# Kernel tuning notes

Measured on AMD Instinct MI355X. Metric: run time of the kernel, lower is better.

The kernel has to match this reference:

```python
import jax, jax.numpy as jnp
import numpy as np

N, DIM, OUT, E = 10000, 256, 256, 320000


def setup_inputs() -> dict:
    key = jax.random.key(0)
    ks = jax.random.split(key, 10)
    def w(k, shape):
        fan_in = shape[0]
        return jax.random.normal(k, shape, jnp.float32) * (fan_in ** -0.5)
    return {
        "v_c": jax.random.normal(ks[0], (N, DIM), jnp.float32),
        # row-normalized-ish random adjacency weights so A @ v stays O(1)
        "A": jax.random.uniform(ks[1], (N, N), jnp.float32) * (2.0 / N),
        "src": jax.random.randint(ks[2], (E,), 0, N, jnp.int32),
        "dst": jax.random.randint(ks[3], (E,), 0, N, jnp.int32),
        # ResidualBlock params: lin1 (dim -> 2dim), lin2 (2dim -> dim)
        "W1": w(ks[4], (DIM, 2 * DIM)), "b1": jnp.zeros((2 * DIM,), jnp.float32),
        "W2": w(ks[5], (2 * DIM, DIM)), "b2": jnp.zeros((DIM,), jnp.float32),
        # LatticeMP_Block lin1 / lin2 (dim -> out_dim)
        "Wl1": w(ks[6], (DIM, OUT)), "bl1": jnp.zeros((OUT,), jnp.float32),
        "Wl2": w(ks[7], (DIM, OUT)), "bl2": jnp.zeros((OUT,), jnp.float32),
    }


def reference(v_c, A, src, dst, W1, b1, W2, b2, Wl1, bl1, Wl2, bl2):
    # ResidualBlock: relu(h + lin2(relu(lin1(h))))
    h1 = jnp.maximum(v_c @ W1 + b1, 0.0) @ W2 + b2          # [N, DIM]
    v = jnp.maximum(v_c + h1, 0.0)                           # [N, DIM]
    # relu(lin1(v)) + relu(lin2(A @ v))
    v = jnp.maximum(v @ Wl1 + bl1, 0.0) + jnp.maximum((A @ v) @ Wl2 + bl2, 0.0)  # [N, OUT]
    # DGL update_all(copy_u, sum): h_N[d] = sum_{(s,d) in E} v[s]
    h_N = jax.ops.segment_sum(v[src], dst, num_segments=N)   # [N, OUT]
    return h_N + v
```

## Files before the change

kernel.cpp:

```cpp
#include <hip/hip_runtime.h>
#include <stdint.h>

#define NN 10000
#define DIMV 256
#define HID 512
#define NEDGE 320000
#define SPLIT 6
#define KCH 1664
#define NKT 313
#define APL 2112
#define ABUF 8448
#define BOFF 16896
#define LDSZ 49664

typedef __attribute__((ext_vector_type(8))) short bf16x8;
typedef __attribute__((ext_vector_type(4))) float f32x4;
typedef __attribute__((ext_vector_type(4))) unsigned short u16x4;
typedef __attribute__((ext_vector_type(2))) unsigned int u32x2;

__device__ __forceinline__ unsigned short f2bf(float f) {
  union { float f; unsigned int u; } c; c.f = f;
  return (unsigned short)((c.u + 0x7FFFu + ((c.u >> 16) & 1u)) >> 16);
}
__device__ __forceinline__ float bf2f(unsigned short h) {
  union { unsigned int u; float f; } c; c.u = ((unsigned int)h) << 16;
  return c.f;
}

__device__ __forceinline__ bf16x8 bzero8() {
  bf16x8 r;
#pragma unroll
  for (int i = 0; i < 8; ++i) r[i] = 0;
  return r;
}

__device__ __forceinline__ bf16x8 pack8(const float* x) {
  bf16x8 r;
#pragma unroll
  for (int i = 0; i < 8; ++i) r[i] = (short)f2bf(x[i]);
  return r;
}

__device__ __forceinline__ u32x2 cvt4v(const f32x4 a) {
  u32x2 r;
  asm("v_cvt_pk_bf16_f32 %0, %1, %2" : "=v"(r[0]) : "v"(a[0]), "v"(a[1]));
  asm("v_cvt_pk_bf16_f32 %0, %1, %2" : "=v"(r[1]) : "v"(a[2]), "v"(a[3]));
  return r;
}

typedef __attribute__((address_space(1))) unsigned int gu32;
typedef __attribute__((address_space(3))) unsigned int lu32;
__device__ __forceinline__ void glds16(const void* g, void* l) {
  __builtin_amdgcn_global_load_lds((const gu32*)g, (lu32*)l, 16, 0, 0);
}

__global__ void k_conv(const float* __restrict__ W1, const float* __restrict__ W2,
                       const float* __restrict__ Wl1, const float* __restrict__ Wl2,
                       unsigned short* __restrict__ W1T, unsigned short* __restrict__ W2T,
                       unsigned short* __restrict__ Wl1T, unsigned short* __restrict__ Wl2T,
                       unsigned short* __restrict__ vB, int* __restrict__ counts) {
  int i = blockIdx.x * 256 + threadIdx.x;
  if (i < 131072) {
    { int k = i >> 9, o = i & 511; W1T[o * 256 + k] = f2bf(W1[i]); }
    { int k = i >> 8, o = i & 255; W2T[o * 512 + k] = f2bf(W2[i]); }
    if (i < 65536) {
      int k = i >> 8, o = i & 255;
      Wl1T[o * 256 + k] = f2bf(Wl1[i]);
      Wl2T[o * 256 + k] = f2bf(Wl2[i]);
    }
    if (i < 4096) {
      int c = i >> 4, kk = 16 + (i & 15);
      int g = kk >> 3;
      int byte = c * 64 + ((g ^ ((c >> 1) & 3)) << 4) + (kk & 7) * 2;
      *(unsigned short*)((char*)vB + (size_t)312 * 16384 + byte) = 0;
    }
    if (i < NN) counts[i] = 0;
  }
}

__launch_bounds__(256, 2)
__global__ void k_mlp(const float* __restrict__ vc,
                      const unsigned short* __restrict__ W1T, const float* __restrict__ b1,
                      const unsigned short* __restrict__ W2T, const float* __restrict__ b2,
                      unsigned short* __restrict__ v_rm, unsigned short* __restrict__ vB,
                      const int* __restrict__ dst, int* __restrict__ counts) {
  if (blockIdx.x >= 313) {
    const int e0 = (blockIdx.x - 313) * 256 + threadIdx.x;
    for (int e = e0; e < NEDGE; e += 40 * 256) atomicAdd(&counts[dst[e]], 1);
    return;
  }
  __shared__ __align__(16) char sm[65536];
  const int t = threadIdx.x;
  const int lane = t & 63, wid = t >> 6;
  const int wr = wid & 1, wc = wid >> 1;
  const int r0 = blockIdx.x * 32;

  {
    const int row = t >> 3, grow = r0 + row;
#pragma unroll
    for (int q = 0; q < 4; ++q) {
      const int slot = (t & 7) * 4 + q;
      float buf[8] = {0.f, 0.f, 0.f, 0.f, 0.f, 0.f, 0.f, 0.f};
      if (grow < NN) {
        const float4 x0 = *(const float4*)(vc + (size_t)grow * DIMV + slot * 8);
        const float4 x1 = *(const float4*)(vc + (size_t)grow * DIMV + slot * 8 + 4);
        buf[0] = x0.x; buf[1] = x0.y; buf[2] = x0.z; buf[3] = x0.w;
        buf[4] = x1.x; buf[5] = x1.y; buf[6] = x1.z; buf[7] = x1.w;
      }
      *(bf16x8*)(sm + row * 512 + ((slot ^ (row & 7)) * 16)) = pack8(buf);
    }
  }

  f32x4 acc1[16];
#pragma unroll
  for (int i = 0; i < 16; ++i) acc1[i] = (f32x4){0.f, 0.f, 0.f, 0.f};

  for (int step = 0; step < 8; ++step) {
    __syncthreads();
#pragma unroll
    for (int rr = 0; rr < 2; ++rr) {
      const int c = t + rr * 256;
      const unsigned short* srcp = W1T + c * 256 + step * 32;
#pragma unroll
      for (int q = 0; q < 4; ++q) {
        bf16x8 w = *(const bf16x8*)(srcp + q * 8);
        *(bf16x8*)(sm + 16384 + c * 64 + ((q ^ ((c >> 1) & 3)) * 16)) = w;
      }
    }
    __syncthreads();
    const int arow = 16 * wr + (lane & 15);
    const int aslot = step * 4 + (lane >> 4);
    const bf16x8 af = *(const bf16x8*)(sm + arow * 512 + ((aslot ^ (arow & 7)) * 16));
#pragma unroll
    for (int ct = 0; ct < 16; ++ct) {
      const int c = 256 * wc + 16 * ct + (lane & 15);
      const bf16x8 bfr =
          *(const bf16x8*)(sm + 16384 + c * 64 + ((((lane >> 4)) ^ ((c >> 1) & 3)) * 16));
      acc1[ct] = __builtin_amdgcn_mfma_f32_16x16x32_bf16(af, bfr, acc1[ct], 0, 0, 0);
    }
  }
  __syncthreads();
#pragma unroll
  for (int ct = 0; ct < 16; ++ct) {
    const int c = 256 * wc + 16 * ct + (lane & 15);
    const float bb = b1[c];
#pragma unroll
    for (int r = 0; r < 4; ++r) {
      const int row = 16 * wr + (lane >> 4) * 4 + r;
      float v = fmaxf(acc1[ct][r] + bb, 0.f);
      const int slot = c >> 3;
      *(unsigned short*)(sm + 16384 + row * 1024 + ((slot ^ (row & 7)) * 16) + (c & 7) * 2) =
          f2bf(v);
    }
  }

  f32x4 acc2[8];
#pragma unroll
  for (int i = 0; i < 8; ++i) acc2[i] = (f32x4){0.f, 0.f, 0.f, 0.f};

  for (int step = 0; step < 16; ++step) {
    __syncthreads();
    {
      const int c = t;
      const unsigned short* srcp = W2T + c * 512 + step * 32;
#pragma unroll
      for (int q = 0; q < 4; ++q) {
        bf16x8 w = *(const bf16x8*)(srcp + q * 8);
        *(bf16x8*)(sm + 49152 + c * 64 + ((q ^ ((c >> 1) & 3)) * 16)) = w;
      }
    }
    __syncthreads();
    const int arow = 16 * wr + (lane & 15);
    const int aslot = step * 4 + (lane >> 4);
    const bf16x8 af = *(const bf16x8*)(sm + 16384 + arow * 1024 + ((aslot ^ (arow & 7)) * 16));
#pragma unroll
    for (int ct = 0; ct < 8; ++ct) {
      const int c = 128 * wc + 16 * ct + (lane & 15);
      const bf16x8 bfr =
          *(const bf16x8*)(sm + 49152 + c * 64 + ((((lane >> 4)) ^ ((c >> 1) & 3)) * 16));
      acc2[ct] = __builtin_amdgcn_mfma_f32_16x16x32_bf16(af, bfr, acc2[ct], 0, 0, 0);
    }
  }

  const int growbase = r0 + 16 * wr + (lane >> 4) * 4;
  if (growbase < NN) {
#pragma unroll
    for (int ct = 0; ct < 8; ++ct) {
      const int c = 128 * wc + 16 * ct + (lane & 15);
      const float bb = b2[c];
      u16x4 pk;
#pragma unroll
      for (int r = 0; r < 4; ++r) {
        const int grow = growbase + r;
        float v = acc2[ct][r] + bb + vc[(size_t)grow * DIMV + c];
        v = fmaxf(v, 0.f);
        const unsigned short hv = f2bf(v);
        v_rm[(size_t)grow * DIMV + c] = hv;
        pk[r] = hv;
      }
      const int tile = growbase >> 5, kk0 = growbase & 31;
      const int g = kk0 >> 3;
      const int byte = c * 64 + ((g ^ ((c >> 1) & 3)) << 4) + (kk0 & 7) * 2;
      *(u16x4*)((char*)vB + (size_t)tile * 16384 + byte) = pk;
    }
  }
}

__launch_bounds__(512, 4)
__global__ void k_av(const float* __restrict__ A, const unsigned short* __restrict__ vB,
                     unsigned short* __restrict__ avpb,
                     const int* __restrict__ counts, int* __restrict__ offsets,
                     int* __restrict__ cursor) {
  __shared__ __align__(16) char sm[LDSZ];
  const int t = threadIdx.x, lane = t & 63, wid = t >> 6;

  if (blockIdx.x >= 474) {
    int* wred = (int*)sm;
    int carry = 0;
    for (int base = 0; base < NN; base += 512) {
      const int i = base + t;
      const int x = (i < NN) ? counts[i] : 0;
      int v = x;
#pragma unroll
      for (int d = 1; d < 64; d <<= 1) {
        int y = __shfl_up(v, d);
        if (lane >= d) v += y;
      }
      if (lane == 63) wred[wid] = v;
      __syncthreads();
      if (t < 8) {
        int sv = wred[t];
#pragma unroll
        for (int d = 1; d < 8; d <<= 1) {
          int y = __shfl_up(sv, d);
          if (t >= d) sv += y;
        }
        wred[t] = sv;
      }
      __syncthreads();
      const int excl = carry + (wid ? wred[wid - 1] : 0) + v - x;
      if (i < NN) { offsets[i] = excl; cursor[i] = excl; }
      carry += wred[7];
      __syncthreads();
    }
    if (t == 0) offsets[NN] = carry;
    return;
  }

  const int wr = wid >> 2, wc = wid & 3;

  const int orig = blockIdx.x;
  const int xcd = orig & 7, idx = orig >> 3;
  const int g = (xcd < 2) ? xcd * 60 + idx : 120 + (xcd - 2) * 59 + idx;
  const int s = g / 79;
  const int xb = g - s * 79;
  const int r0 = xb * 128;
  const int kbase = s * KCH;
  const int tile0 = s * 52;
  const int nst = (s == SPLIT - 1) ? 53 : 52;
  unsigned short* outp = avpb + (size_t)s * NN * DIMV;

  const int srow = t >> 3, sQ = t & 7;
  const float* ap0 = A + (size_t)min(r0 + srow, NN - 1) * NN;
  const float* ap1 = A + (size_t)min(r0 + 64 + srow, NN - 1) * NN;
  const int wbase = (sQ >> 1) * APL + (sQ & 1) * 8;
  const int w0 = wbase + srow * 16;
  const int w1 = wbase + (64 + srow) * 16;

  f32x4 aR0, aR1;

#define AISSUE(ST)                                            \
  do {                                                        \
    int kq = kbase + (ST)*32 + sQ * 4;                        \
    kq = min(kq, 9996);         \
    aR0 = *(const f32x4*)(ap0 + kq);                          \
    aR1 = *(const f32x4*)(ap1 + kq);                          \
  } while (0)

#define AWRITE(BUF)                                           \
  do {                                                        \
    char* wb = sm + (BUF)*ABUF;                               \
    *(u32x2*)(wb + w0) = cvt4v(aR0);                          \
    *(u32x2*)(wb + w1) = cvt4v(aR1);                          \
  } while (0)

#define BSTAGE(BUF, TILE)                                                     \
  do {                                                                        \
    char* lb = sm + BOFF + (BUF)*16384 + wid * 1024;                          \
    const char* gp = (const char*)vB + (size_t)(TILE)*16384 + wid * 1024 +    \
                     lane * 16;                                               \
    glds16(gp, lb);                                                           \
    glds16(gp + 8192, lb + 8192);                                             \
  } while (0)

  f32x4 acc[4][4];
#pragma unroll
  for (int i = 0; i < 4; ++i)
#pragma unroll
    for (int j = 0; j < 4; ++j) acc[i][j] = (f32x4){0.f, 0.f, 0.f, 0.f};

  const int rbase = (lane >> 4) * APL + (wr * 64 + (lane & 15)) * 16;
  int boff[4];
#pragma unroll
  for (int ct = 0; ct < 4; ++ct) {
    const int col = wc * 64 + ct * 16 + (lane & 15);
    boff[ct] = col * 64 + (((lane >> 4) ^ ((col >> 1) & 3)) << 4);
  }

#define COMPUTE(CUR)                                                                 \
  do {                                                                              \
    const char* ab = sm + (CUR)*ABUF;                                               \
    const char* bb = sm + BOFF + (CUR)*16384;                                       \
    const bf16x8 af0 = *(const bf16x8*)(ab + rbase);                                \
    const bf16x8 af1 = *(const bf16x8*)(ab + rbase + 256);                          \
    const bf16x8 af2 = *(const bf16x8*)(ab + rbase + 512);                          \
    const bf16x8 af3 = *(const bf16x8*)(ab + rbase + 768);                          \
    _Pragma("unroll") for (int ct = 0; ct < 4; ++ct) {                              \
      const bf16x8 bfr = *(const bf16x8*)(bb + boff[ct]);                           \
      acc[0][ct] = __builtin_amdgcn_mfma_f32_16x16x32_bf16(af0, bfr, acc[0][ct], 0, 0, 0); \
      acc[1][ct] = __builtin_amdgcn_mfma_f32_16x16x32_bf16(af1, bfr, acc[1][ct], 0, 0, 0); \
      acc[2][ct] = __builtin_amdgcn_mfma_f32_16x16x32_bf16(af2, bfr, acc[2][ct], 0, 0, 0); \
      acc[3][ct] = __builtin_amdgcn_mfma_f32_16x16x32_bf16(af3, bfr, acc[3][ct], 0, 0, 0); \
    }                                                                               \
  } while (0)

  AISSUE(0);
  AWRITE(0);
  BSTAGE(0, tile0);
  __syncthreads();

  int cur = 0;
  for (int st = 0; st < nst; ++st) {
    const bool more = (st + 1 < nst);
    if (more) {
      AISSUE(st + 1);
      BSTAGE(cur ^ 1, tile0 + st + 1);
    }
    COMPUTE(cur);
    if (more) AWRITE(cur ^ 1);
    __syncthreads();
    cur ^= 1;
  }
#undef AISSUE
#undef AWRITE
#undef BSTAGE
#undef COMPUTE

#pragma unroll
  for (int rt = 0; rt < 4; ++rt) {
    const int gb = r0 + wr * 64 + rt * 16 + (lane >> 4) * 4;
    if (gb < NN) {
#pragma unroll
      for (int ct = 0; ct < 4; ++ct) {
        const int col = wc * 64 + ct * 16 + (lane & 15);
#pragma unroll
        for (int r = 0; r < 4; ++r)
          outp[(size_t)(gb + r) * DIMV + col] = f2bf(acc[rt][ct][r]);
      }
    }
  }
}

__launch_bounds__(256, 2)
__global__ void k_out(const unsigned short* __restrict__ v_rm,
                      const unsigned short* __restrict__ avpb,
                      const unsigned short* __restrict__ Wl1T, const float* __restrict__ bl1,
                      const unsigned short* __restrict__ Wl2T, const float* __restrict__ bl2,
                      unsigned short* __restrict__ v2b, float* __restrict__ outb,
                      const int* __restrict__ src, const int* __restrict__ dst,
                      int* __restrict__ cursor, int* __restrict__ srcbuf) {
  if (blockIdx.x >= 313) {
    const int e0 = (blockIdx.x - 313) * 256 + threadIdx.x;
    for (int e = e0; e < NEDGE; e += 40 * 256) {
      const int pos = atomicAdd(&cursor[dst[e]], 1);
      srcbuf[pos] = src[e];
    }
    return;
  }
  __shared__ __align__(16) char sm[65536];
  const int t = threadIdx.x, lane = t & 63, wid = t >> 6;
  const int wr = wid & 1, wc = wid >> 1;
  const int r0 = blockIdx.x * 32;

  {
    const int row = t >> 3, grow = r0 + row;
#pragma unroll
    for (int q = 0; q < 4; ++q) {
      const int slot = (t & 7) * 4 + q;
      bf16x8 w = (grow < NN) ? *(const bf16x8*)(v_rm + (size_t)grow * DIMV + slot * 8) : bzero8();
      *(bf16x8*)(sm + row * 512 + ((slot ^ (row & 7)) * 16)) = w;
    }
#pragma unroll
    for (int q = 0; q < 4; ++q) {
      const int slot = (t & 7) * 4 + q;
      float buf[8] = {0.f, 0.f, 0.f, 0.f, 0.f, 0.f, 0.f, 0.f};
      if (grow < NN) {
#pragma unroll
        for (int p = 0; p < SPLIT; ++p) {
          const bf16x8 a =
              *(const bf16x8*)(avpb + (size_t)p * NN * DIMV + (size_t)grow * DIMV + slot * 8);
#pragma unroll
          for (int z = 0; z < 8; ++z) buf[z] += bf2f((unsigned short)a[z]);
        }
      }
      *(bf16x8*)(sm + 16384 + row * 512 + ((slot ^ (row & 7)) * 16)) = pack8(buf);
    }
  }

  f32x4 acc1[8], acc2[8];
#pragma unroll
  for (int i = 0; i < 8; ++i) {
    acc1[i] = (f32x4){0.f, 0.f, 0.f, 0.f};
    acc2[i] = (f32x4){0.f, 0.f, 0.f, 0.f};
  }

  for (int step = 0; step < 8; ++step) {
    __syncthreads();
    {
      const int c = t;
      const unsigned short* s1 = Wl1T + c * 256 + step * 32;
      const unsigned short* s2 = Wl2T + c * 256 + step * 32;
#pragma unroll
      for (int q = 0; q < 4; ++q) {
        const int ps = (q ^ ((c >> 1) & 3)) * 16;
        *(bf16x8*)(sm + 32768 + c * 64 + ps) = *(const bf16x8*)(s1 + q * 8);
        *(bf16x8*)(sm + 49152 + c * 64 + ps) = *(const bf16x8*)(s2 + q * 8);
      }
    }
    __syncthreads();
    const int arow = 16 * wr + (lane & 15);
    const int aslot = step * 4 + (lane >> 4);
    const bf16x8 a1 = *(const bf16x8*)(sm + arow * 512 + ((aslot ^ (arow & 7)) * 16));
    const bf16x8 a2 = *(const bf16x8*)(sm + 16384 + arow * 512 + ((aslot ^ (arow & 7)) * 16));
#pragma unroll
    for (int ct = 0; ct < 8; ++ct) {
      const int c = 128 * wc + 16 * ct + (lane & 15);
      const int bs = (((lane >> 4)) ^ ((c >> 1) & 3)) * 16;
      acc1[ct] = __builtin_amdgcn_mfma_f32_16x16x32_bf16(
          a1, *(const bf16x8*)(sm + 32768 + c * 64 + bs), acc1[ct], 0, 0, 0);
      acc2[ct] = __builtin_amdgcn_mfma_f32_16x16x32_bf16(
          a2, *(const bf16x8*)(sm + 49152 + c * 64 + bs), acc2[ct], 0, 0, 0);
    }
  }

  const int growbase = r0 + 16 * wr + (lane >> 4) * 4;
  if (growbase < NN) {
#pragma unroll
    for (int ct = 0; ct < 8; ++ct) {
      const int c = 128 * wc + 16 * ct + (lane & 15);
      const float u1 = bl1[c], u2 = bl2[c];
#pragma unroll
      for (int r = 0; r < 4; ++r) {
        const float x = fmaxf(acc1[ct][r] + u1, 0.f) + fmaxf(acc2[ct][r] + u2, 0.f);
        v2b[(size_t)(growbase + r) * DIMV + c] = f2bf(x);
        outb[(size_t)(growbase + r) * DIMV + c] = x;
      }
    }
  }
}

__launch_bounds__(256)
__global__ void k_gather(const unsigned short* __restrict__ v2b,
                         const int* __restrict__ offsets,
                         const int* __restrict__ srcbuf, float* __restrict__ outb) {
  const int n = (blockIdx.x * 256 + threadIdx.x) >> 6;
  if (n >= NN) return;
  const int lane = threadIdx.x & 63;
  const int beg = offsets[n], end = offsets[n + 1];
  float4 a0 = {0.f, 0.f, 0.f, 0.f}, a1 = a0, a2 = a0, a3 = a0;
  float4 a4 = a0, a5 = a0, a6 = a0, a7 = a0;
  int j = beg;
  for (; j + 8 <= end; j += 8) {
    const int s0 = srcbuf[j], s1 = srcbuf[j + 1], s2 = srcbuf[j + 2], s3 = srcbuf[j + 3];
    const int s4 = srcbuf[j + 4], s5 = srcbuf[j + 5], s6 = srcbuf[j + 6], s7 = srcbuf[j + 7];
    const u16x4 x0 = *(const u16x4*)(v2b + (size_t)s0 * DIMV + lane * 4);
    const u16x4 x1 = *(const u16x4*)(v2b + (size_t)s1 * DIMV + lane * 4);
    const u16x4 x2 = *(const u16x4*)(v2b + (size_t)s2 * DIMV + lane * 4);
    const u16x4 x3 = *(const u16x4*)(v2b + (size_t)s3 * DIMV + lane * 4);
    const u16x4 x4 = *(const u16x4*)(v2b + (size_t)s4 * DIMV + lane * 4);
    const u16x4 x5 = *(const u16x4*)(v2b + (size_t)s5 * DIMV + lane * 4);
    const u16x4 x6 = *(const u16x4*)(v2b + (size_t)s6 * DIMV + lane * 4);
    const u16x4 x7 = *(const u16x4*)(v2b + (size_t)s7 * DIMV + lane * 4);
    a0.x += bf2f(x0[0]); a0.y += bf2f(x0[1]); a0.z += bf2f(x0[2]); a0.w += bf2f(x0[3]);
    a1.x += bf2f(x1[0]); a1.y += bf2f(x1[1]); a1.z += bf2f(x1[2]); a1.w += bf2f(x1[3]);
    a2.x += bf2f(x2[0]); a2.y += bf2f(x2[1]); a2.z += bf2f(x2[2]); a2.w += bf2f(x2[3]);
    a3.x += bf2f(x3[0]); a3.y += bf2f(x3[1]); a3.z += bf2f(x3[2]); a3.w += bf2f(x3[3]);
    a4.x += bf2f(x4[0]); a4.y += bf2f(x4[1]); a4.z += bf2f(x4[2]); a4.w += bf2f(x4[3]);
    a5.x += bf2f(x5[0]); a5.y += bf2f(x5[1]); a5.z += bf2f(x5[2]); a5.w += bf2f(x5[3]);
    a6.x += bf2f(x6[0]); a6.y += bf2f(x6[1]); a6.z += bf2f(x6[2]); a6.w += bf2f(x6[3]);
    a7.x += bf2f(x7[0]); a7.y += bf2f(x7[1]); a7.z += bf2f(x7[2]); a7.w += bf2f(x7[3]);
  }
  for (; j < end; ++j) {
    const int s0 = srcbuf[j];
    const u16x4 x0 = *(const u16x4*)(v2b + (size_t)s0 * DIMV + lane * 4);
    a0.x += bf2f(x0[0]); a0.y += bf2f(x0[1]); a0.z += bf2f(x0[2]); a0.w += bf2f(x0[3]);
  }
  a0.x += a1.x + a2.x + a3.x + a4.x + a5.x + a6.x + a7.x;
  a0.y += a1.y + a2.y + a3.y + a4.y + a5.y + a6.y + a7.y;
  a0.z += a1.z + a2.z + a3.z + a4.z + a5.z + a6.z + a7.z;
  a0.w += a1.w + a2.w + a3.w + a4.w + a5.w + a6.w + a7.w;
  float* o = outb + (size_t)n * DIMV + lane * 4;
  float4 cur = *(const float4*)o;
  cur.x += a0.x; cur.y += a0.y; cur.z += a0.z; cur.w += a0.w;
  *(float4*)o = cur;
}

extern "C" void kernel_launch(void* const* d_in, const int* in_sizes, int n_in,
                              void* d_out, int out_size, void* d_ws, size_t ws_size,
                              hipStream_t stream) {
  const float* vc  = (const float*)d_in[0];
  const float* A   = (const float*)d_in[1];
  const int*   src = (const int*)d_in[2];
  const int*   dst = (const int*)d_in[3];
  const float* W1  = (const float*)d_in[4];
  const float* b1  = (const float*)d_in[5];
  const float* W2  = (const float*)d_in[6];
  const float* b2  = (const float*)d_in[7];
  const float* Wl1 = (const float*)d_in[8];
  const float* bl1 = (const float*)d_in[9];
  const float* Wl2 = (const float*)d_in[10];
  const float* bl2 = (const float*)d_in[11];
  float* outb = (float*)d_out;
  char* ws = (char*)d_ws;

  unsigned short* W1T  = (unsigned short*)(ws + 0);
  unsigned short* W2T  = (unsigned short*)(ws + 262144);
  unsigned short* Wl1T = (unsigned short*)(ws + 524288);
  unsigned short* Wl2T = (unsigned short*)(ws + 655360);
  unsigned short* vB   = (unsigned short*)(ws + 786432);
  unsigned short* v_rm = (unsigned short*)(ws + 5914624);
  int* counts  = (int*)(ws + 11034624);
  int* offsets = (int*)(ws + 11075584);
  int* cursor  = (int*)(ws + 11116544);
  int* srcbuf  = (int*)(ws + 11157504);
  unsigned short* avpb = (unsigned short*)(ws + 12437760);
  unsigned short* v2b  = (unsigned short*)(ws + 43157760);

  hipLaunchKernelGGL(k_conv, dim3(512), dim3(256), 0, stream,
                     W1, W2, Wl1, Wl2, W1T, W2T, Wl1T, Wl2T, vB, counts);
  hipLaunchKernelGGL(k_mlp, dim3(353), dim3(256), 0, stream,
                     vc, W1T, b1, W2T, b2, v_rm, vB, dst, counts);
  hipLaunchKernelGGL(k_av, dim3(475), dim3(512), 0, stream,
                     A, vB, avpb, counts, offsets, cursor);
  hipLaunchKernelGGL(k_out, dim3(353), dim3(256), 0, stream,
                     v_rm, avpb, Wl1T, bl1, Wl2T, bl2, v2b, outb,
                     src, dst, cursor, srcbuf);
  hipLaunchKernelGGL(k_gather, dim3((NN * 64 + 255) / 256), dim3(256), 0, stream,
                     v2b, offsets, srcbuf, outb);
}
```

Baseline: 236.6 us.

## Stage fp32 A tiles via direct-to-LDS loads with triple buffering in A@v GEMM

The A@v kernel now loads fp32 A tiles straight into LDS with global_load_lds (XOR-swizzled) and converts them to bf16 at fragment-read time, instead of loading into registers and writing converted values. It switches to a 3-stage ring buffer with explicit vmcnt waits and raw barriers. Row tiles shrink from 128 to 64, doubling the block count to 942 with a matching XCD remap. The aim is to hide the HBM stream of A better and drop register staging, at the cost of more LDS per block (72KB), reading A from LDS in fp32, and halving MFMA reuse per B fragment.

```diff
diff --git a/kernel.cpp b/kernel.cpp
--- a/kernel.cpp
+++ b/kernel.cpp
@@ -8,10 +8,8 @@
 #define SPLIT 6
 #define KCH 1664
 #define NKT 313
-#define APL 2112
-#define ABUF 8448
-#define BOFF 16896
-#define LDSZ 49664
+#define BUFSZ 24576
+#define NGEMM 942
 
 typedef __attribute__((ext_vector_type(8))) short bf16x8;
 typedef __attribute__((ext_vector_type(4))) float f32x4;
@@ -41,11 +39,13 @@
   return r;
 }
 
-__device__ __forceinline__ u32x2 cvt4v(const f32x4 a) {
-  u32x2 r;
-  asm("v_cvt_pk_bf16_f32 %0, %1, %2" : "=v"(r[0]) : "v"(a[0]), "v"(a[1]));
-  asm("v_cvt_pk_bf16_f32 %0, %1, %2" : "=v"(r[1]) : "v"(a[2]), "v"(a[3]));
-  return r;
+__device__ __forceinline__ bf16x8 cvt8v(const f32x4 a, const f32x4 b) {
+  union { unsigned int u[4]; bf16x8 v; } r;
+  asm("v_cvt_pk_bf16_f32 %0, %1, %2" : "=v"(r.u[0]) : "v"(a[0]), "v"(a[1]));
+  asm("v_cvt_pk_bf16_f32 %0, %1, %2" : "=v"(r.u[1]) : "v"(a[2]), "v"(a[3]));
+  asm("v_cvt_pk_bf16_f32 %0, %1, %2" : "=v"(r.u[2]) : "v"(b[0]), "v"(b[1]));
+  asm("v_cvt_pk_bf16_f32 %0, %1, %2" : "=v"(r.u[3]) : "v"(b[2]), "v"(b[3]));
+  return r.v;
 }
 
 typedef __attribute__((address_space(1))) unsigned int gu32;
@@ -211,10 +211,10 @@
                      unsigned short* __restrict__ avpb,
                      const int* __restrict__ counts, int* __restrict__ offsets,
                      int* __restrict__ cursor) {
-  __shared__ __align__(16) char sm[LDSZ];
+  __shared__ __align__(16) char sm[73728];
   const int t = threadIdx.x, lane = t & 63, wid = t >> 6;
 
-  if (blockIdx.x >= 474) {
+  if (blockIdx.x >= NGEMM) {
     int* wred = (int*)sm;
     int carry = 0;
     for (int base = 0; base < NN; base += 512) {
@@ -251,104 +251,90 @@
 
   const int orig = blockIdx.x;
   const int xcd = orig & 7, idx = orig >> 3;
-  const int g = (xcd < 2) ? xcd * 60 + idx : 120 + (xcd - 2) * 59 + idx;
-  const int s = g / 79;
-  const int xb = g - s * 79;
-  const int r0 = xb * 128;
+  const int g = (xcd < 6) ? xcd * 118 + idx : 708 + (xcd - 6) * 117 + idx;
+  const int s = g / 157;
+  const int xb = g - s * 157;
+  const int r0 = xb * 64;
   const int kbase = s * KCH;
   const int tile0 = s * 52;
   const int nst = (s == SPLIT - 1) ? 53 : 52;
   unsigned short* outp = avpb + (size_t)s * NN * DIMV;
 
-  const int srow = t >> 3, sQ = t & 7;
-  const float* ap0 = A + (size_t)min(r0 + srow, NN - 1) * NN;
-  const float* ap1 = A + (size_t)min(r0 + 64 + srow, NN - 1) * NN;
-  const int wbase = (sQ >> 1) * APL + (sQ & 1) * 8;
-  const int w0 = wbase + srow * 16;
-  const int w1 = wbase + (64 + srow) * 16;
-
-  f32x4 aR0, aR1;
-
-#define AISSUE(ST)                                            \
-  do {                                                        \
-    int kq = kbase + (ST)*32 + sQ * 4;                        \
-    kq = min(kq, 9996);         \
-    aR0 = *(const f32x4*)(ap0 + kq);                          \
-    aR1 = *(const f32x4*)(ap1 + kq);                          \
+  const int arow_t = wid * 8 + (lane >> 3);
+  const int ac4 = ((lane & 7) ^ (lane >> 3)) * 4;
+  const float* abase_g = A + (size_t)min(r0 + arow_t, NN - 1) * NN;
+
+#define GSTAGE(BI, ST)                                                         \
+  do {                                                                         \
+    char* la_ = sm + (BI)*BUFSZ + wid * 1024;                                  \
+    const float* ga_ = abase_g + min(kbase + (ST)*32 + ac4, 9996);             \
+    glds16(ga_, la_);                                                          \
+    char* lb_ = sm + (BI)*BUFSZ + 8192 + wid * 1024;                           \
+    const char* gb_ =                                                          \
+        (const char*)vB + (size_t)(tile0 + (ST)) * 16384 + wid * 1024 + lane * 16; \
+    glds16(gb_, lb_);                                                          \
+    glds16(gb_ + 8192, lb_ + 8192);                                            \
   } while (0)
 
-#define AWRITE(BUF)                                           \
-  do {                                                        \
-    char* wb = sm + (BUF)*ABUF;                               \
-    *(u32x2*)(wb + w0) = cvt4v(aR0);                          \
-    *(u32x2*)(wb + w1) = cvt4v(aR1);                          \
-  } while (0)
-
-#define BSTAGE(BUF, TILE)                                                     \
-  do {                                                                        \
-    char* lb = sm + BOFF + (BUF)*16384 + wid * 1024;                          \
-    const char* gp = (const char*)vB + (size_t)(TILE)*16384 + wid * 1024 +    \
-                     lane * 16;                                               \
-    glds16(gp, lb);                                                           \
-    glds16(gp + 8192, lb + 8192);                                             \
-  } while (0)
-
-  f32x4 acc[4][4];
-#pragma unroll
-  for (int i = 0; i < 4; ++i)
+  f32x4 acc[2][4];
+#pragma unroll
+  for (int i = 0; i < 2; ++i)
 #pragma unroll
     for (int j = 0; j < 4; ++j) acc[i][j] = (f32x4){0.f, 0.f, 0.f, 0.f};
 
-  const int rbase = (lane >> 4) * APL + (wr * 64 + (lane & 15)) * 16;
+  const int frow = wr * 32 + (lane & 15);
+  const int kg = lane >> 4;
   int boff[4];
 #pragma unroll
   for (int ct = 0; ct < 4; ++ct) {
     const int col = wc * 64 + ct * 16 + (lane & 15);
-    boff[ct] = col * 64 + (((lane >> 4) ^ ((col >> 1) & 3)) << 4);
-  }
-
-#define COMPUTE(CUR)                                                                 \
-  do {                                                                              \
-    const char* ab = sm + (CUR)*ABUF;                                               \
-    const char* bb = sm + BOFF + (CUR)*16384;                                       \
-    const bf16x8 af0 = *(const bf16x8*)(ab + rbase);                                \
-    const bf16x8 af1 = *(const bf16x8*)(ab + rbase + 256);                          \
-    const bf16x8 af2 = *(const bf16x8*)(ab + rbase + 512);                          \
-    const bf16x8 af3 = *(const bf16x8*)(ab + rbase + 768);                          \
-    _Pragma("unroll") for (int ct = 0; ct < 4; ++ct) {                              \
-      const bf16x8 bfr = *(const bf16x8*)(bb + boff[ct]);                           \
+    boff[ct] = 8192 + col * 64 + ((kg ^ ((col >> 1) & 3)) << 4);
+  }
+
+#define COMPUTE(BI)                                                            \
+  do {                                                                         \
+    const char* bb_ = sm + (BI)*BUFSZ;                                         \
+    const int rw_ = frow & 7;                                                  \
+    const bf16x8 af0 = cvt8v(                                                  \
+        *(const f32x4*)(bb_ + frow * 128 + (((kg * 2) ^ rw_) << 4)),           \
+        *(const f32x4*)(bb_ + frow * 128 + (((kg * 2 + 1) ^ rw_) << 4)));      \
+    const bf16x8 af1 = cvt8v(                                                  \
+        *(const f32x4*)(bb_ + (frow + 16) * 128 + (((kg * 2) ^ rw_) << 4)),    \
+        *(const f32x4*)(bb_ + (frow + 16) * 128 + (((kg * 2 + 1) ^ rw_) << 4)));\
+    _Pragma("unroll") for (int ct = 0; ct < 4; ++ct) {                         \
+      const bf16x8 bfr = *(const bf16x8*)(bb_ + boff[ct]);                     \
       acc[0][ct] = __builtin_amdgcn_mfma_f32_16x16x32_bf16(af0, bfr, acc[0][ct], 0, 0, 0); \
       acc[1][ct] = __builtin_amdgcn_mfma_f32_16x16x32_bf16(af1, bfr, acc[1][ct], 0, 0, 0); \
-      acc[2][ct] = __builtin_amdgcn_mfma_f32_16x16x32_bf16(af2, bfr, acc[2][ct], 0, 0, 0); \
-      acc[3][ct] = __builtin_amdgcn_mfma_f32_16x16x32_bf16(af3, bfr, acc[3][ct], 0, 0, 0); \
-    }                                                                               \
+    }                                                                          \
   } while (0)
 
-  AISSUE(0);
-  AWRITE(0);
-  BSTAGE(0, tile0);
-  __syncthreads();
+  GSTAGE(0, 0);
+  GSTAGE(1, 1);
 
   int cur = 0;
   for (int st = 0; st < nst; ++st) {
-    const bool more = (st + 1 < nst);
-    if (more) {
-      AISSUE(st + 1);
-      BSTAGE(cur ^ 1, tile0 + st + 1);
-    }
+    if (st + 2 < nst) {
+      int sb = cur + 2; if (sb >= 3) sb -= 3;
+      GSTAGE(sb, st + 2);
+    }
+    __builtin_amdgcn_sched_barrier(0);
+    const int ahead = nst - 1 - st;
+    if (ahead >= 2)      asm volatile("s_waitcnt vmcnt(6)" ::: "memory");
+    else if (ahead == 1) asm volatile("s_waitcnt vmcnt(3)" ::: "memory");
+    else                 asm volatile("s_waitcnt vmcnt(0)" ::: "memory");
+    __builtin_amdgcn_sched_barrier(0);
+    __builtin_amdgcn_s_barrier();
     COMPUTE(cur);
-    if (more) AWRITE(cur ^ 1);
-    __syncthreads();
-    cur ^= 1;
-  }
-#undef AISSUE
-#undef AWRITE
-#undef BSTAGE
+    __builtin_amdgcn_sched_barrier(0);
+    __builtin_amdgcn_s_barrier();
+    ++cur; if (cur >= 3) cur = 0;
+  }
+#undef GSTAGE
 #undef COMPUTE
 
 #pragma unroll
-  for (int rt = 0; rt < 4; ++rt) {
-    const int gb = r0 + wr * 64 + rt * 16 + (lane >> 4) * 4;
+  for (int rt = 0; rt < 2; ++rt) {
+    const int gb = r0 + wr * 32 + rt * 16 + (lane >> 4) * 4;
     if (gb < NN) {
 #pragma unroll
       for (int ct = 0; ct < 4; ++ct) {
@@ -540,7 +526,7 @@
                      W1, W2, Wl1, Wl2, W1T, W2T, Wl1T, Wl2T, vB, counts);
   hipLaunchKernelGGL(k_mlp, dim3(353), dim3(256), 0, stream,
                      vc, W1T, b1, W2T, b2, v_rm, vB, dst, counts);
-  hipLaunchKernelGGL(k_av, dim3(475), dim3(512), 0, stream,
+  hipLaunchKernelGGL(k_av, dim3(NGEMM + 1), dim3(512), 0, stream,
                      A, vB, avpb, counts, offsets, cursor);
   hipLaunchKernelGGL(k_out, dim3(353), dim3(256), 0, stream,
                      v_rm, avpb, Wl1T, bl1, Wl2T, bl2, v2b, outb,
```

After: 257.5 us. +8.8%, slower.

## Prefetch A-tile global loads two stages ahead with register double-buffering

Applied to the files above, without the earlier changes.

The A-operand global loads in the split-K GEMM now go into two alternating register sets and are issued two stages ahead of use, instead of one. Explicit s_waitcnt vmcnt(2) plus a raw s_barrier replace __syncthreads, so the newest A loads can stay in flight across the barrier. This is meant to hide HBM latency on the streaming reads of the large A matrix. The cost is extra VGPRs and fragile hand-written wait counts that assume the compiler's memory-op ordering.

```diff
diff --git a/kernel.cpp b/kernel.cpp
--- a/kernel.cpp
+++ b/kernel.cpp
@@ -267,21 +267,31 @@
   const int w0 = wbase + srow * 16;
   const int w1 = wbase + (64 + srow) * 16;
 
-  f32x4 aR0, aR1;
-
-#define AISSUE(ST)                                            \
+  f32x4 aR0, aR1, bR0, bR1;
+
+#define AISSUE_A(ST)                                          \
   do {                                                        \
-    int kq = kbase + (ST)*32 + sQ * 4;                        \
-    kq = min(kq, 9996);         \
+    int kq = min(kbase + (ST)*32 + sQ * 4, 9996);             \
     aR0 = *(const f32x4*)(ap0 + kq);                          \
     aR1 = *(const f32x4*)(ap1 + kq);                          \
   } while (0)
-
-#define AWRITE(BUF)                                           \
+#define AISSUE_B(ST)                                          \
+  do {                                                        \
+    int kq = min(kbase + (ST)*32 + sQ * 4, 9996);             \
+    bR0 = *(const f32x4*)(ap0 + kq);                          \
+    bR1 = *(const f32x4*)(ap1 + kq);                          \
+  } while (0)
+#define AWRITE_A(BUF)                                         \
   do {                                                        \
     char* wb = sm + (BUF)*ABUF;                               \
     *(u32x2*)(wb + w0) = cvt4v(aR0);                          \
     *(u32x2*)(wb + w1) = cvt4v(aR1);                          \
+  } while (0)
+#define AWRITE_B(BUF)                                         \
+  do {                                                        \
+    char* wb = sm + (BUF)*ABUF;                               \
+    *(u32x2*)(wb + w0) = cvt4v(bR0);                          \
+    *(u32x2*)(wb + w1) = cvt4v(bR1);                          \
   } while (0)
 
 #define BSTAGE(BUF, TILE)                                                     \
@@ -307,42 +317,57 @@
     boff[ct] = col * 64 + (((lane >> 4) ^ ((col >> 1) & 3)) << 4);
   }
 
-#define COMPUTE(CUR)                                                                 \
-  do {                                                                              \
-    const char* ab = sm + (CUR)*ABUF;                                               \
-    const char* bb = sm + BOFF + (CUR)*16384;                                       \
-    const bf16x8 af0 = *(const bf16x8*)(ab + rbase);                                \
-    const bf16x8 af1 = *(const bf16x8*)(ab + rbase + 256);                          \
-    const bf16x8 af2 = *(const bf16x8*)(ab + rbase + 512);                          \
-    const bf16x8 af3 = *(const bf16x8*)(ab + rbase + 768);                          \
-    _Pragma("unroll") for (int ct = 0; ct < 4; ++ct) {                              \
-      const bf16x8 bfr = *(const bf16x8*)(bb + boff[ct]);                           \
+#define COMPUTE(CUR)                                                               \
+  do {                                                                            \
+    const char* ab = sm + (CUR)*ABUF;                                             \
+    const char* bb = sm + BOFF + (CUR)*16384;                                     \
+    const bf16x8 af0 = *(const bf16x8*)(ab + rbase);                              \
+    const bf16x8 af1 = *(const bf16x8*)(ab + rbase + 256);                        \
+    const bf16x8 af2 = *(const bf16x8*)(ab + rbase + 512);                        \
+    const bf16x8 af3 = *(const bf16x8*)(ab + rbase + 768);                        \
+    _Pragma("unroll") for (int ct = 0; ct < 4; ++ct) {                            \
+      const bf16x8 bfr = *(const bf16x8*)(bb + boff[ct]);                         \
       acc[0][ct] = __builtin_amdgcn_mfma_f32_16x16x32_bf16(af0, bfr, acc[0][ct], 0, 0, 0); \
       acc[1][ct] = __builtin_amdgcn_mfma_f32_16x16x32_bf16(af1, bfr, acc[1][ct], 0, 0, 0); \
       acc[2][ct] = __builtin_amdgcn_mfma_f32_16x16x32_bf16(af2, bfr, acc[2][ct], 0, 0, 0); \
       acc[3][ct] = __builtin_amdgcn_mfma_f32_16x16x32_bf16(af3, bfr, acc[3][ct], 0, 0, 0); \
-    }                                                                               \
+    }                                                                             \
   } while (0)
 
-  AISSUE(0);
-  AWRITE(0);
+  AISSUE_A(0);
+  AWRITE_A(0);
   BSTAGE(0, tile0);
-  __syncthreads();
+  AISSUE_B(1);
+  __builtin_amdgcn_sched_barrier(0);
+  asm volatile("s_waitcnt lgkmcnt(0)" ::: "memory");
+  asm volatile("s_waitcnt vmcnt(2)" ::: "memory");
+  __builtin_amdgcn_sched_barrier(0);
+  __builtin_amdgcn_s_barrier();
 
   int cur = 0;
   for (int st = 0; st < nst; ++st) {
     const bool more = (st + 1 < nst);
+    const bool more2 = (st + 2 < nst);
+    if (more) BSTAGE(cur ^ 1, tile0 + st + 1);
+    if (more2) {
+      if ((st & 1) == 0) AISSUE_A(st + 2); else AISSUE_B(st + 2);
+    }
+    COMPUTE(cur);
     if (more) {
-      AISSUE(st + 1);
-      BSTAGE(cur ^ 1, tile0 + st + 1);
-    }
-    COMPUTE(cur);
-    if (more) AWRITE(cur ^ 1);
-    __syncthreads();
+      if ((st & 1) == 0) AWRITE_B(cur ^ 1); else AWRITE_A(cur ^ 1);
+    }
+    __builtin_amdgcn_sched_barrier(0);
+    asm volatile("s_waitcnt lgkmcnt(0)" ::: "memory");
+    if (more2) asm volatile("s_waitcnt vmcnt(2)" ::: "memory");
+    else       asm volatile("s_waitcnt vmcnt(0)" ::: "memory");
+    __builtin_amdgcn_sched_barrier(0);
+    __builtin_amdgcn_s_barrier();
     cur ^= 1;
   }
-#undef AISSUE
-#undef AWRITE
+#undef AISSUE_A
+#undef AISSUE_B
+#undef AWRITE_A
+#undef AWRITE_B
 #undef BSTAGE
 #undef COMPUTE
 
```

New measurement: 239.5 us. Within noise of the previous version (+1.2%).

## Pre-tile weights into MFMA fragment order and read B operands directly from global

Applied to the files above, without the earlier changes.

The weight conversion kernel now writes W1/W2/Wl1/Wl2 in a k-tiled, fragment-contiguous layout so each lane's 16-byte MFMA B operand sits contiguously in global memory. The MLP and post-aggregation kernels then load B fragments straight from global/L2 instead of staging them through LDS each k-step. This removes two barriers per step and shrinks LDS use, which may raise occupancy. The trade-off is exposed global-load latency on every MFMA operand, with no LDS reuse across waves.

```diff
diff --git a/kernel.cpp b/kernel.cpp
--- a/kernel.cpp
+++ b/kernel.cpp
@@ -61,12 +61,19 @@
                        unsigned short* __restrict__ vB, int* __restrict__ counts) {
   int i = blockIdx.x * 256 + threadIdx.x;
   if (i < 131072) {
-    { int k = i >> 9, o = i & 511; W1T[o * 256 + k] = f2bf(W1[i]); }
-    { int k = i >> 8, o = i & 255; W2T[o * 512 + k] = f2bf(W2[i]); }
+    {
+      int tile = i >> 14, o = (i >> 5) & 511, kk = i & 31;
+      W1T[i] = f2bf(W1[(size_t)(tile * 32 + kk) * 512 + o]);
+    }
+    {
+      int tile = i >> 13, o = (i >> 5) & 255, kk = i & 31;
+      W2T[i] = f2bf(W2[(size_t)(tile * 32 + kk) * 256 + o]);
+    }
     if (i < 65536) {
-      int k = i >> 8, o = i & 255;
-      Wl1T[o * 256 + k] = f2bf(Wl1[i]);
-      Wl2T[o * 256 + k] = f2bf(Wl2[i]);
+      int tile = i >> 13, o = (i >> 5) & 255, kk = i & 31;
+      int srci = (tile * 32 + kk) * 256 + o;
+      Wl1T[i] = f2bf(Wl1[srci]);
+      Wl2T[i] = f2bf(Wl2[srci]);
     }
     if (i < 4096) {
       int c = i >> 4, kk = 16 + (i & 15);
@@ -89,7 +96,7 @@
     for (int e = e0; e < NEDGE; e += 40 * 256) atomicAdd(&counts[dst[e]], 1);
     return;
   }
-  __shared__ __align__(16) char sm[65536];
+  __shared__ __align__(16) char sm[49152];
   const int t = threadIdx.x;
   const int lane = t & 63, wid = t >> 6;
   const int wr = wid & 1, wc = wid >> 1;
@@ -110,36 +117,26 @@
       *(bf16x8*)(sm + row * 512 + ((slot ^ (row & 7)) * 16)) = pack8(buf);
     }
   }
+  __syncthreads();
 
   f32x4 acc1[16];
 #pragma unroll
   for (int i = 0; i < 16; ++i) acc1[i] = (f32x4){0.f, 0.f, 0.f, 0.f};
 
+#pragma unroll 1
   for (int step = 0; step < 8; ++step) {
-    __syncthreads();
-#pragma unroll
-    for (int rr = 0; rr < 2; ++rr) {
-      const int c = t + rr * 256;
-      const unsigned short* srcp = W1T + c * 256 + step * 32;
-#pragma unroll
-      for (int q = 0; q < 4; ++q) {
-        bf16x8 w = *(const bf16x8*)(srcp + q * 8);
-        *(bf16x8*)(sm + 16384 + c * 64 + ((q ^ ((c >> 1) & 3)) * 16)) = w;
-      }
-    }
-    __syncthreads();
     const int arow = 16 * wr + (lane & 15);
     const int aslot = step * 4 + (lane >> 4);
     const bf16x8 af = *(const bf16x8*)(sm + arow * 512 + ((aslot ^ (arow & 7)) * 16));
+    const unsigned short* wb = W1T + step * 16384 + (lane & 15) * 32 + (lane >> 4) * 8;
 #pragma unroll
     for (int ct = 0; ct < 16; ++ct) {
-      const int c = 256 * wc + 16 * ct + (lane & 15);
-      const bf16x8 bfr =
-          *(const bf16x8*)(sm + 16384 + c * 64 + ((((lane >> 4)) ^ ((c >> 1) & 3)) * 16));
+      const int c0 = 256 * wc + 16 * ct;
+      const bf16x8 bfr = *(const bf16x8*)(wb + c0 * 32);
       acc1[ct] = __builtin_amdgcn_mfma_f32_16x16x32_bf16(af, bfr, acc1[ct], 0, 0, 0);
     }
   }
-  __syncthreads();
+
 #pragma unroll
   for (int ct = 0; ct < 16; ++ct) {
     const int c = 256 * wc + 16 * ct + (lane & 15);
@@ -153,31 +150,22 @@
           f2bf(v);
     }
   }
+  __syncthreads();
 
   f32x4 acc2[8];
 #pragma unroll
   for (int i = 0; i < 8; ++i) acc2[i] = (f32x4){0.f, 0.f, 0.f, 0.f};
 
+#pragma unroll 1
   for (int step = 0; step < 16; ++step) {
-    __syncthreads();
-    {
-      const int c = t;
-      const unsigned short* srcp = W2T + c * 512 + step * 32;
-#pragma unroll
-      for (int q = 0; q < 4; ++q) {
-        bf16x8 w = *(const bf16x8*)(srcp + q * 8);
-        *(bf16x8*)(sm + 49152 + c * 64 + ((q ^ ((c >> 1) & 3)) * 16)) = w;
-      }
-    }
-    __syncthreads();
     const int arow = 16 * wr + (lane & 15);
     const int aslot = step * 4 + (lane >> 4);
     const bf16x8 af = *(const bf16x8*)(sm + 16384 + arow * 1024 + ((aslot ^ (arow & 7)) * 16));
+    const unsigned short* wb = W2T + step * 8192 + (lane & 15) * 32 + (lane >> 4) * 8;
 #pragma unroll
     for (int ct = 0; ct < 8; ++ct) {
-      const int c = 128 * wc + 16 * ct + (lane & 15);
-      const bf16x8 bfr =
-          *(const bf16x8*)(sm + 49152 + c * 64 + ((((lane >> 4)) ^ ((c >> 1) & 3)) * 16));
+      const int c0 = 128 * wc + 16 * ct;
+      const bf16x8 bfr = *(const bf16x8*)(wb + c0 * 32);
       acc2[ct] = __builtin_amdgcn_mfma_f32_16x16x32_bf16(af, bfr, acc2[ct], 0, 0, 0);
     }
   }
@@ -271,8 +259,7 @@
 
 #define AISSUE(ST)                                            \
   do {                                                        \
-    int kq = kbase + (ST)*32 + sQ * 4;                        \
-    kq = min(kq, 9996);         \
+    int kq = min(kbase + (ST)*32 + sQ * 4, 9996);             \
     aR0 = *(const f32x4*)(ap0 + kq);                          \
     aR1 = *(const f32x4*)(ap1 + kq);                          \
   } while (0)
@@ -307,21 +294,21 @@
     boff[ct] = col * 64 + (((lane >> 4) ^ ((col >> 1) & 3)) << 4);
   }
 
-#define COMPUTE(CUR)                                                                 \
-  do {                                                                              \
-    const char* ab = sm + (CUR)*ABUF;                                               \
-    const char* bb = sm + BOFF + (CUR)*16384;                                       \
-    const bf16x8 af0 = *(const bf16x8*)(ab + rbase);                                \
-    const bf16x8 af1 = *(const bf16x8*)(ab + rbase + 256);                          \
-    const bf16x8 af2 = *(const bf16x8*)(ab + rbase + 512);                          \
-    const bf16x8 af3 = *(const bf16x8*)(ab + rbase + 768);                          \
-    _Pragma("unroll") for (int ct = 0; ct < 4; ++ct) {                              \
-      const bf16x8 bfr = *(const bf16x8*)(bb + boff[ct]);                           \
+#define COMPUTE(CUR)                                                               \
+  do {                                                                            \
+    const char* ab = sm + (CUR)*ABUF;                                             \
+    const char* bb = sm + BOFF + (CUR)*16384;                                     \
+    const bf16x8 af0 = *(const bf16x8*)(ab + rbase);                              \
+    const bf16x8 af1 = *(const bf16x8*)(ab + rbase + 256);                        \
+    const bf16x8 af2 = *(const bf16x8*)(ab + rbase + 512);                        \
+    const bf16x8 af3 = *(const bf16x8*)(ab + rbase + 768);                        \
+    _Pragma("unroll") for (int ct = 0; ct < 4; ++ct) {                            \
+      const bf16x8 bfr = *(const bf16x8*)(bb + boff[ct]);                         \
       acc[0][ct] = __builtin_amdgcn_mfma_f32_16x16x32_bf16(af0, bfr, acc[0][ct], 0, 0, 0); \
       acc[1][ct] = __builtin_amdgcn_mfma_f32_16x16x32_bf16(af1, bfr, acc[1][ct], 0, 0, 0); \
       acc[2][ct] = __builtin_amdgcn_mfma_f32_16x16x32_bf16(af2, bfr, acc[2][ct], 0, 0, 0); \
       acc[3][ct] = __builtin_amdgcn_mfma_f32_16x16x32_bf16(af3, bfr, acc[3][ct], 0, 0, 0); \
-    }                                                                               \
+    }                                                                             \
   } while (0)
 
   AISSUE(0);
@@ -377,7 +364,7 @@
     }
     return;
   }
-  __shared__ __align__(16) char sm[65536];
+  __shared__ __align__(16) char sm[32768];
   const int t = threadIdx.x, lane = t & 63, wid = t >> 6;
   const int wr = wid & 1, wc = wid >> 1;
   const int r0 = blockIdx.x * 32;
@@ -406,6 +393,7 @@
       *(bf16x8*)(sm + 16384 + row * 512 + ((slot ^ (row & 7)) * 16)) = pack8(buf);
     }
   }
+  __syncthreads();
 
   f32x4 acc1[8], acc2[8];
 #pragma unroll
@@ -414,32 +402,21 @@
     acc2[i] = (f32x4){0.f, 0.f, 0.f, 0.f};
   }
 
+#pragma unroll 1
   for (int step = 0; step < 8; ++step) {
-    __syncthreads();
-    {
-      const int c = t;
-      const unsigned short* s1 = Wl1T + c * 256 + step * 32;
-      const unsigned short* s2 = Wl2T + c * 256 + step * 32;
-#pragma unroll
-      for (int q = 0; q < 4; ++q) {
-        const int ps = (q ^ ((c >> 1) & 3)) * 16;
-        *(bf16x8*)(sm + 32768 + c * 64 + ps) = *(const bf16x8*)(s1 + q * 8);
-        *(bf16x8*)(sm + 49152 + c * 64 + ps) = *(const bf16x8*)(s2 + q * 8);
-      }
-    }
-    __syncthreads();
     const int arow = 16 * wr + (lane & 15);
     const int aslot = step * 4 + (lane >> 4);
     const bf16x8 a1 = *(const bf16x8*)(sm + arow * 512 + ((aslot ^ (arow & 7)) * 16));
     const bf16x8 a2 = *(const bf16x8*)(sm + 16384 + arow * 512 + ((aslot ^ (arow & 7)) * 16));
+    const unsigned short* w1p = Wl1T + step * 8192 + (lane & 15) * 32 + (lane >> 4) * 8;
+    const unsigned short* w2p = Wl2T + step * 8192 + (lane & 15) * 32 + (lane >> 4) * 8;
 #pragma unroll
     for (int ct = 0; ct < 8; ++ct) {
-      const int c = 128 * wc + 16 * ct + (lane & 15);
-      const int bs = (((lane >> 4)) ^ ((c >> 1) & 3)) * 16;
+      const int c0 = 128 * wc + 16 * ct;
       acc1[ct] = __builtin_amdgcn_mfma_f32_16x16x32_bf16(
-          a1, *(const bf16x8*)(sm + 32768 + c * 64 + bs), acc1[ct], 0, 0, 0);
+          a1, *(const bf16x8*)(w1p + c0 * 32), acc1[ct], 0, 0, 0);
       acc2[ct] = __builtin_amdgcn_mfma_f32_16x16x32_bf16(
-          a2, *(const bf16x8*)(sm + 49152 + c * 64 + bs), acc2[ct], 0, 0, 0);
+          a2, *(const bf16x8*)(w2p + c0 * 32), acc2[ct], 0, 0, 0);
     }
   }
 
```

Result: no change. 232.9 us (-1.5%).
